# Kernel optimization log

Hardware: AMD Instinct MI355X
Metric: run time of the kernel (lower is better)

Reference implementation:

```python
import jax, jax.numpy as jnp
import numpy as np

D_IN = 1024
D_OUT = 1024
NUM_HEADS = 16
HEAD_DIM = D_OUT // NUM_HEADS

def setup_inputs() -> dict:
    key = jax.random.key(0)
    ks = jax.random.split(key, 6)
    b, t = 2, 2048
    s = 0.02
    return {
        "x": jax.random.normal(ks[0], (b, t, D_IN), dtype=jnp.float32),
        "Wq": jax.random.normal(ks[1], (D_IN, D_OUT), dtype=jnp.float32) * s,
        "Wk": jax.random.normal(ks[2], (D_IN, D_OUT), dtype=jnp.float32) * s,
        "Wv": jax.random.normal(ks[3], (D_IN, D_OUT), dtype=jnp.float32) * s,
        "Wo": jax.random.normal(ks[4], (D_OUT, D_OUT), dtype=jnp.float32) * s,
        "bo": jax.random.normal(ks[5], (D_OUT,), dtype=jnp.float32) * s,
    }

def reference(x, Wq, Wk, Wv, Wo, bo):
    b, t, _ = x.shape
    # QKV projections -> [b, h, t, d]
    def split_heads(y):
        return y.reshape(b, t, NUM_HEADS, HEAD_DIM).transpose(0, 2, 1, 3)
    q = split_heads(x @ Wq)
    k = split_heads(x @ Wk)
    v = split_heads(x @ Wv)
    # scores [b, h, t, t], causal mask, softmax over keys
    scores = jnp.einsum('bhqd,bhkd->bhqk', q, k)
    causal = jnp.tril(jnp.ones((t, t), dtype=bool))  # True where allowed
    scores = jnp.where(causal, scores, -jnp.inf)
    attn = jax.nn.softmax(scores / jnp.sqrt(jnp.float32(HEAD_DIM)), axis=-1)
    ctx = jnp.einsum('bhqk,bhkd->bhqd', attn, v)
    ctx = ctx.transpose(0, 2, 1, 3).reshape(b, t, D_OUT)
    return ctx @ Wo + bo
```

## Files before the change

### kernel.cpp

```cpp
#include <hip/hip_runtime.h>
#include <hip/hip_bf16.h>
#include <cstdint>
#include <cstddef>


typedef __bf16 bf16_t;
typedef __bf16 bf16x2 __attribute__((ext_vector_type(2)));
typedef __bf16 bf16x8 __attribute__((ext_vector_type(8)));
typedef float  f32x4  __attribute__((ext_vector_type(4)));

#define B_SZ 2
#define T_SZ 2048
#define DIN  1024
#define NH   16
#define HD   64

#define SCL_Q (0.125f * 1.44269504088896f)

__device__ __forceinline__ void gld_lds16(const void* g, void* l) {
    __builtin_amdgcn_global_load_lds(
        (const __attribute__((address_space(1))) void*)g,
        (__attribute__((address_space(3))) void*)l,
        16, 0, 0);
}

__global__ __launch_bounds__(256) void cvt_x_kernel(const float* __restrict__ src,
                                                    bf16_t* __restrict__ dst) {
    int i = blockIdx.x * blockDim.x + threadIdx.x;
    size_t base = (size_t)i * 8;
    float4 a = *(const float4*)(src + base);
    float4 b = *(const float4*)(src + base + 4);
    bf16x8 v;
    v[0] = (bf16_t)a.x; v[1] = (bf16_t)a.y; v[2] = (bf16_t)a.z; v[3] = (bf16_t)a.w;
    v[4] = (bf16_t)b.x; v[5] = (bf16_t)b.y; v[6] = (bf16_t)b.z; v[7] = (bf16_t)b.w;
    *(bf16x8*)(dst + base) = v;
}

__global__ __launch_bounds__(256) void transpose_cvt_kernel(const float* __restrict__ src,
                                                            bf16_t* __restrict__ dst,
                                                            int R, int C) {
    __shared__ float tile[32][33];
    int c0 = blockIdx.x * 32, r0 = blockIdx.y * 32;
    int tx = threadIdx.x, ty = threadIdx.y;
#pragma unroll
    for (int i = 0; i < 32; i += 8)
        tile[ty + i][tx] = src[(size_t)(r0 + ty + i) * C + c0 + tx];
    __syncthreads();
#pragma unroll
    for (int i = 0; i < 32; i += 8)
        dst[(size_t)(c0 + ty + i) * R + r0 + tx] = (bf16_t)tile[tx][ty + i];
}

__device__ __forceinline__ void gemm_tile_body(const bf16_t* __restrict__ A,
                                               const bf16_t* __restrict__ Bt,
                                               int m0, int n0, int K,
                                               f32x4 acc[4][4],
                                               bf16_t* As, bf16_t* Bs) {
    const int tid  = threadIdx.x;
    const int lane = tid & 63;
    const int wave = tid >> 6;
    const int wr   = (wave >> 1) * 64;
    const int wc   = (wave & 1) * 64;

#pragma unroll
    for (int mi = 0; mi < 4; ++mi)
#pragma unroll
        for (int ni = 0; ni < 4; ++ni)
            acc[mi][ni] = (f32x4){0.f, 0.f, 0.f, 0.f};

    for (int k0 = 0; k0 < K; k0 += 32) {
#pragma unroll
        for (int c = 0; c < 2; ++c) {
            int fb = (wave * 2 + c) * 1024;
            int e  = (fb >> 1) + lane * 8;
            int r  = e >> 5;
            int kk = e & 31;
            gld_lds16(A  + (size_t)(m0 + r) * K + k0 + kk, (char*)As + fb);
            gld_lds16(Bt + (size_t)(n0 + r) * K + k0 + kk, (char*)Bs + fb);
        }
        __syncthreads();

        bf16x8 af[4], bfr[4];
#pragma unroll
        for (int mi = 0; mi < 4; ++mi)
            af[mi] = *(const bf16x8*)(As + (wr + mi * 16 + (lane & 15)) * 32 + ((lane >> 4) * 8));
#pragma unroll
        for (int ni = 0; ni < 4; ++ni)
            bfr[ni] = *(const bf16x8*)(Bs + (wc + ni * 16 + (lane & 15)) * 32 + ((lane >> 4) * 8));
#pragma unroll
        for (int mi = 0; mi < 4; ++mi)
#pragma unroll
            for (int ni = 0; ni < 4; ++ni)
                acc[mi][ni] = __builtin_amdgcn_mfma_f32_16x16x32_bf16(af[mi], bfr[ni], acc[mi][ni], 0, 0, 0);
        __syncthreads();
    }
}

__global__ __launch_bounds__(256, 2) void gemm_qkv_kernel(const bf16_t* __restrict__ A,
                                                          const bf16_t* __restrict__ Bt,
                                                          bf16_t* __restrict__ Qb,
                                                          bf16_t* __restrict__ Kb,
                                                          bf16_t* __restrict__ Vt) {
    __shared__ alignas(16) bf16_t As[128 * 32];
    __shared__ alignas(16) bf16_t Bs[128 * 32];
    const int nTn = 3072 / 128;
    int m0 = (blockIdx.x / nTn) * 128;
    int n0 = (blockIdx.x % nTn) * 128;
    f32x4 acc[4][4];
    gemm_tile_body(A, Bt, m0, n0, DIN, acc, As, Bs);

    const int lane = threadIdx.x & 63;
    const int wave = threadIdx.x >> 6;
    const int wr = (wave >> 1) * 64, wc = (wave & 1) * 64;
#pragma unroll
    for (int mi = 0; mi < 4; ++mi)
#pragma unroll
        for (int ni = 0; ni < 4; ++ni)
#pragma unroll
            for (int j = 0; j < 4; ++j) {
                int m = m0 + wr + mi * 16 + ((lane >> 4) * 4) + j;
                int n = n0 + wc + ni * 16 + (lane & 15);
                int b = m >> 11, t = m & 2047;
                int part = n >> 10, c = n & 1023;
                int h = c >> 6, d = c & 63;
                float av = acc[mi][ni][j];
                if (part == 0)
                    Qb[(((size_t)(b * NH + h) * T_SZ + t) << 6) + d] = (bf16_t)(av * SCL_Q);
                else if (part == 1)
                    Kb[(((size_t)(b * NH + h) * T_SZ + t) << 6) + d] = (bf16_t)av;
                else
                    Vt[((size_t)(b * NH + h) * HD + d) * T_SZ + t] = (bf16_t)av;
            }
}

__global__ __launch_bounds__(256, 3) void attn_kernel(const bf16_t* __restrict__ Qb,
                                                      const bf16_t* __restrict__ Kb,
                                                      const bf16_t* __restrict__ Vt,
                                                      bf16_t* __restrict__ ctx) {
    __shared__ alignas(16) bf16_t Ks[2][64 * 64];
    __shared__ alignas(16) bf16_t Vs[2][64 * 64];
    __shared__ alignas(16) bf16_t P_lds[4][16][72];

    const int raw = blockIdx.x;
    const int xcd = raw & 7;
    const int jj  = raw >> 3;
    const int bh  = xcd * 4 + (jj & 3);
    const int qt  = 31 - (jj >> 2);

    const int lane = threadIdx.x & 63;
    const int wave = threadIdx.x >> 6;

    const bf16_t* Qp = Qb + (size_t)bh * T_SZ * HD;
    const bf16_t* Kp = Kb + (size_t)bh * T_SZ * HD;
    const bf16_t* Vp = Vt + (size_t)bh * HD * T_SZ;

    const int q0 = qt * 64 + wave * 16;
    const int rgrp = lane >> 4;
    const int rcol = lane & 15;

    const int st_r  = (lane >> 3);
    const int st_sl = lane & 7;

    bf16x8 qa[2];
#pragma unroll
    for (int s = 0; s < 2; ++s)
        qa[s] = *(const bf16x8*)(Qp + (size_t)(q0 + rcol) * HD + s * 32 + rgrp * 8);

    f32x4 o[4];
#pragma unroll
    for (int di = 0; di < 4; ++di) o[di] = (f32x4){0.f, 0.f, 0.f, 0.f};
    float mrun = -__builtin_inff();
    float lrun = 0.f;

#define STAGE(BUF, KT)                                                          \
    {                                                                           \
        const int k0s = (KT) * 64;                                              \
        _Pragma("unroll")                                                       \
        for (int c = 0; c < 2; ++c) {                                           \
            int r0 = (wave * 2 + c) * 8;                                        \
            int r  = r0 + st_r;                                                 \
            int sl = st_sl ^ (r & 7);                                           \
            gld_lds16(Kp + (size_t)(k0s + r) * HD + sl * 8,                     \
                      (char*)&Ks[BUF][0] + r0 * 128);                           \
            gld_lds16(Vp + (size_t)r * T_SZ + k0s + sl * 8,                     \
                      (char*)&Vs[BUF][0] + r0 * 128);                           \
        }                                                                       \
    }

    STAGE(0, 0);
    __syncthreads();
    int buf = 0;

    for (int kt = 0; kt <= qt; ++kt) {
        if (kt < qt) STAGE(buf ^ 1, kt + 1);

        const char* Kb_l = (const char*)&Ks[buf][0];
        const char* Vb_l = (const char*)&Vs[buf][0];

        f32x4 s_acc[4];
#pragma unroll
        for (int ni = 0; ni < 4; ++ni) s_acc[ni] = (f32x4){0.f, 0.f, 0.f, 0.f};
#pragma unroll
        for (int s = 0; s < 2; ++s)
#pragma unroll
            for (int ni = 0; ni < 4; ++ni) {
                int fr = ni * 16 + rcol;
                bf16x8 kb = *(const bf16x8*)(Kb_l + fr * 128 + (((s * 4 + rgrp) ^ (fr & 7)) << 4));
                s_acc[ni] = __builtin_amdgcn_mfma_f32_16x16x32_bf16(kb, qa[s], s_acc[ni], 0, 0, 0);
            }

        bf16x8 vf[2][4];
#pragma unroll
        for (int s = 0; s < 2; ++s)
#pragma unroll
            for (int di = 0; di < 4; ++di) {
                int fv = di * 16 + rcol;
                vf[s][di] = *(const bf16x8*)(Vb_l + fv * 128 + (((s * 4 + rgrp) ^ (fv & 7)) << 4));
            }

        float ptile[4][4];
        float pmax = -__builtin_inff();
        if (kt == qt) {
            const int qabs = q0 + rcol;
#pragma unroll
            for (int ni = 0; ni < 4; ++ni)
#pragma unroll
                for (int j = 0; j < 4; ++j) {
                    int kidx = qt * 64 + ni * 16 + rgrp * 4 + j;
                    float v = s_acc[ni][j];
                    if (kidx > qabs) v = -__builtin_inff();
                    ptile[ni][j] = v;
                    pmax = fmaxf(pmax, v);
                }
        } else {
#pragma unroll
            for (int ni = 0; ni < 4; ++ni)
#pragma unroll
                for (int j = 0; j < 4; ++j) {
                    float v = s_acc[ni][j];
                    ptile[ni][j] = v;
                    pmax = fmaxf(pmax, v);
                }
        }
        pmax = fmaxf(pmax, __shfl_xor(pmax, 16));
        pmax = fmaxf(pmax, __shfl_xor(pmax, 32));

        const bool fullb = __any(pmax > mrun + 8.f);
        float a_self = 1.f;
        if (fullb) {
            float newm = fmaxf(mrun, pmax);
            a_self = exp2f(mrun - newm);
            mrun = newm;
        }
        float rsum = 0.f;
#pragma unroll
        for (int ni = 0; ni < 4; ++ni)
#pragma unroll
            for (int j = 0; j < 4; ++j) {
                float p = exp2f(ptile[ni][j] - mrun);
                ptile[ni][j] = p;
                rsum += p;
            }
        rsum += __shfl_xor(rsum, 16);
        rsum += __shfl_xor(rsum, 32);
        if (fullb) {
            lrun = lrun * a_self + rsum;
#pragma unroll
            for (int j = 0; j < 4; ++j) {
                float aj = __shfl(a_self, (lane & 48) | (rgrp * 4 + j));
#pragma unroll
                for (int di = 0; di < 4; ++di) o[di][j] *= aj;
            }
        } else {
            lrun += rsum;
        }

#pragma unroll
        for (int ni = 0; ni < 4; ++ni)
#pragma unroll
            for (int jp = 0; jp < 2; ++jp) {
                bf16x2 pk;
                pk[0] = (bf16_t)ptile[ni][2 * jp];
                pk[1] = (bf16_t)ptile[ni][2 * jp + 1];
                *(bf16x2*)&P_lds[wave][rcol][ni * 16 + rgrp * 4 + 2 * jp] = pk;
            }
#pragma unroll
        for (int s = 0; s < 2; ++s) {
            bf16x8 pa = *(const bf16x8*)(&P_lds[wave][rcol][s * 32 + rgrp * 8]);
#pragma unroll
            for (int di = 0; di < 4; ++di)
                o[di] = __builtin_amdgcn_mfma_f32_16x16x32_bf16(pa, vf[s][di], o[di], 0, 0, 0);
        }
        __syncthreads();
        buf ^= 1;
    }
#undef STAGE

    const int b = bh >> 4, h = bh & 15;
    float invl[4];
#pragma unroll
    for (int j = 0; j < 4; ++j) {
        float lj = __shfl(lrun, (lane & 48) | (rgrp * 4 + j));
        invl[j] = 1.f / lj;
    }
#pragma unroll
    for (int di = 0; di < 4; ++di)
#pragma unroll
        for (int j = 0; j < 4; ++j) {
            int q = q0 + rgrp * 4 + j;
            int d = di * 16 + rcol;
            ctx[((size_t)(b * T_SZ + q) * NH + h) * HD + d] = (bf16_t)(o[di][j] * invl[j]);
        }
}

__global__ __launch_bounds__(256, 2) void gemm_out_kernel(const bf16_t* __restrict__ A,
                                                          const bf16_t* __restrict__ Bt,
                                                          const float* __restrict__ bias,
                                                          float* __restrict__ out) {
    __shared__ alignas(16) bf16_t As[128 * 32];
    __shared__ alignas(16) bf16_t Bs[128 * 32];
    const int nTn = 1024 / 128;
    int m0 = (blockIdx.x / nTn) * 128;
    int n0 = (blockIdx.x % nTn) * 128;
    f32x4 acc[4][4];
    gemm_tile_body(A, Bt, m0, n0, DIN, acc, As, Bs);

    const int lane = threadIdx.x & 63;
    const int wave = threadIdx.x >> 6;
    const int wr = (wave >> 1) * 64, wc = (wave & 1) * 64;
#pragma unroll
    for (int mi = 0; mi < 4; ++mi)
#pragma unroll
        for (int ni = 0; ni < 4; ++ni) {
            int n = n0 + wc + ni * 16 + (lane & 15);
            float bv = bias[n];
#pragma unroll
            for (int j = 0; j < 4; ++j) {
                int m = m0 + wr + mi * 16 + ((lane >> 4) * 4) + j;
                out[(size_t)m * 1024 + n] = acc[mi][ni][j] + bv;
            }
        }
}

extern "C" void kernel_launch(void* const* d_in, const int* in_sizes, int n_in,
                              void* d_out, int out_size, void* d_ws, size_t ws_size,
                              hipStream_t stream) {
    const float* x  = (const float*)d_in[0];
    const float* Wq = (const float*)d_in[1];
    const float* Wk = (const float*)d_in[2];
    const float* Wv = (const float*)d_in[3];
    const float* Wo = (const float*)d_in[4];
    const float* bo = (const float*)d_in[5];
    float* out = (float*)d_out;

    char* ws = (char*)d_ws;
    bf16_t* x_bf   = (bf16_t*)(ws);
    bf16_t* Wqkv_t = (bf16_t*)(ws + ((size_t)8 << 20));
    bf16_t* Wo_t   = (bf16_t*)(ws + ((size_t)14 << 20));
    bf16_t* Qb     = (bf16_t*)(ws + ((size_t)16 << 20));
    bf16_t* Kb     = (bf16_t*)(ws + ((size_t)24 << 20));
    bf16_t* Vt     = (bf16_t*)(ws + ((size_t)32 << 20));
    bf16_t* ctx    = (bf16_t*)(ws + ((size_t)40 << 20));

    cvt_x_kernel<<<2048, 256, 0, stream>>>(x, x_bf);
    transpose_cvt_kernel<<<dim3(32, 32), dim3(32, 8), 0, stream>>>(Wq, Wqkv_t, 1024, 1024);
    transpose_cvt_kernel<<<dim3(32, 32), dim3(32, 8), 0, stream>>>(Wk, Wqkv_t + (size_t)1024 * 1024, 1024, 1024);
    transpose_cvt_kernel<<<dim3(32, 32), dim3(32, 8), 0, stream>>>(Wv, Wqkv_t + (size_t)2048 * 1024, 1024, 1024);
    transpose_cvt_kernel<<<dim3(32, 32), dim3(32, 8), 0, stream>>>(Wo, Wo_t, 1024, 1024);
    gemm_qkv_kernel<<<32 * 24, 256, 0, stream>>>(x_bf, Wqkv_t, Qb, Kb, Vt);
    attn_kernel<<<B_SZ * NH * 32, 256, 0, stream>>>(Qb, Kb, Vt, ctx);
    gemm_out_kernel<<<32 * 8, 256, 0, stream>>>(ctx, Wo_t, bo, out);
}
```

Before: 194.7 us.

## Fuse prep kernels, remap GEMM blocks per XCD, vectorize V stores, shrink out-GEMM tile

Merges the x conversion and four weight transpose launches into one prep kernel to cut launch overhead. Remaps the QKV and output GEMM block indices so that neighbouring tiles are grouped onto the same XCD, which should improve L2 reuse. Stores V-transpose outputs as 4-wide vectors instead of scalar scattered writes. Halves the output GEMM M tile to 64 rows, doubling its grid from 256 to 512 blocks and raising the occupancy bound to 3, so the 256 CUs are filled better at the cost of less reuse per tile.

After: 174.9 us. -10.2%, faster.

```diff
diff --git a/kernel.cpp b/kernel.cpp
--- a/kernel.cpp
+++ b/kernel.cpp
@@ -6,6 +6,7 @@
 
 typedef __bf16 bf16_t;
 typedef __bf16 bf16x2 __attribute__((ext_vector_type(2)));
+typedef __bf16 bf16x4 __attribute__((ext_vector_type(4)));
 typedef __bf16 bf16x8 __attribute__((ext_vector_type(8)));
 typedef float  f32x4  __attribute__((ext_vector_type(4)));
 
@@ -24,31 +25,41 @@
         16, 0, 0);
 }
 
-__global__ __launch_bounds__(256) void cvt_x_kernel(const float* __restrict__ src,
-                                                    bf16_t* __restrict__ dst) {
-    int i = blockIdx.x * blockDim.x + threadIdx.x;
-    size_t base = (size_t)i * 8;
-    float4 a = *(const float4*)(src + base);
-    float4 b = *(const float4*)(src + base + 4);
-    bf16x8 v;
-    v[0] = (bf16_t)a.x; v[1] = (bf16_t)a.y; v[2] = (bf16_t)a.z; v[3] = (bf16_t)a.w;
-    v[4] = (bf16_t)b.x; v[5] = (bf16_t)b.y; v[6] = (bf16_t)b.z; v[7] = (bf16_t)b.w;
-    *(bf16x8*)(dst + base) = v;
-}
-
-__global__ __launch_bounds__(256) void transpose_cvt_kernel(const float* __restrict__ src,
-                                                            bf16_t* __restrict__ dst,
-                                                            int R, int C) {
+__global__ __launch_bounds__(256) void prep_kernel(const float* __restrict__ x,
+                                                   bf16_t* __restrict__ x_bf,
+                                                   const float* __restrict__ Wq,
+                                                   const float* __restrict__ Wk,
+                                                   const float* __restrict__ Wv,
+                                                   const float* __restrict__ Wo,
+                                                   bf16_t* __restrict__ Wqkv_t,
+                                                   bf16_t* __restrict__ Wo_t) {
     __shared__ float tile[32][33];
-    int c0 = blockIdx.x * 32, r0 = blockIdx.y * 32;
-    int tx = threadIdx.x, ty = threadIdx.y;
+    const int bid = blockIdx.x;
+    const int tid = threadIdx.x;
+    if (bid < 2048) {
+        size_t base = ((size_t)bid * 256 + tid) * 8;
+        float4 a = *(const float4*)(x + base);
+        float4 b = *(const float4*)(x + base + 4);
+        bf16x8 v;
+        v[0] = (bf16_t)a.x; v[1] = (bf16_t)a.y; v[2] = (bf16_t)a.z; v[3] = (bf16_t)a.w;
+        v[4] = (bf16_t)b.x; v[5] = (bf16_t)b.y; v[6] = (bf16_t)b.z; v[7] = (bf16_t)b.w;
+        *(bf16x8*)(x_bf + base) = v;
+        return;
+    }
+    const int tb = bid - 2048;
+    const int w  = tb >> 10;
+    const int t2 = tb & 1023;
+    const int c0 = (t2 & 31) * 32, r0 = (t2 >> 5) * 32;
+    const float* src = (w == 0) ? Wq : (w == 1) ? Wk : (w == 2) ? Wv : Wo;
+    bf16_t* dst = (w < 3) ? (Wqkv_t + (size_t)w * 1024 * 1024) : Wo_t;
+    const int tx = tid & 31, ty = tid >> 5;
 #pragma unroll
     for (int i = 0; i < 32; i += 8)
-        tile[ty + i][tx] = src[(size_t)(r0 + ty + i) * C + c0 + tx];
+        tile[ty + i][tx] = src[(size_t)(r0 + ty + i) * 1024 + c0 + tx];
     __syncthreads();
 #pragma unroll
     for (int i = 0; i < 32; i += 8)
-        dst[(size_t)(c0 + ty + i) * R + r0 + tx] = (bf16_t)tile[tx][ty + i];
+        dst[(size_t)(c0 + ty + i) * 1024 + r0 + tx] = (bf16_t)tile[tx][ty + i];
 }
 
 __device__ __forceinline__ void gemm_tile_body(const bf16_t* __restrict__ A,
@@ -104,8 +115,9 @@
     __shared__ alignas(16) bf16_t As[128 * 32];
     __shared__ alignas(16) bf16_t Bs[128 * 32];
     const int nTn = 3072 / 128;
-    int m0 = (blockIdx.x / nTn) * 128;
-    int n0 = (blockIdx.x % nTn) * 128;
+    const int bid = (blockIdx.x & 7) * 96 + (blockIdx.x >> 3);
+    int m0 = (bid / nTn) * 128;
+    int n0 = (bid % nTn) * 128;
     f32x4 acc[4][4];
     gemm_tile_body(A, Bt, m0, n0, DIN, acc, As, Bs);
 
@@ -115,22 +127,29 @@
 #pragma unroll
     for (int mi = 0; mi < 4; ++mi)
 #pragma unroll
-        for (int ni = 0; ni < 4; ++ni)
-#pragma unroll
-            for (int j = 0; j < 4; ++j) {
-                int m = m0 + wr + mi * 16 + ((lane >> 4) * 4) + j;
-                int n = n0 + wc + ni * 16 + (lane & 15);
-                int b = m >> 11, t = m & 2047;
-                int part = n >> 10, c = n & 1023;
-                int h = c >> 6, d = c & 63;
-                float av = acc[mi][ni][j];
-                if (part == 0)
-                    Qb[(((size_t)(b * NH + h) * T_SZ + t) << 6) + d] = (bf16_t)(av * SCL_Q);
-                else if (part == 1)
-                    Kb[(((size_t)(b * NH + h) * T_SZ + t) << 6) + d] = (bf16_t)av;
-                else
-                    Vt[((size_t)(b * NH + h) * HD + d) * T_SZ + t] = (bf16_t)av;
-            }
+        for (int ni = 0; ni < 4; ++ni) {
+            int t0 = m0 + wr + mi * 16 + ((lane >> 4) * 4);
+            int n  = n0 + wc + ni * 16 + (lane & 15);
+            int b  = t0 >> 11, tl = t0 & 2047;
+            int part = n >> 10, c = n & 1023;
+            int h = c >> 6, d = c & 63;
+            if (part == 2) {
+                bf16x4 pv;
+#pragma unroll
+                for (int j = 0; j < 4; ++j) pv[j] = (bf16_t)acc[mi][ni][j];
+                *(bf16x4*)&Vt[((size_t)(b * NH + h) * HD + d) * T_SZ + tl] = pv;
+            } else if (part == 0) {
+#pragma unroll
+                for (int j = 0; j < 4; ++j)
+                    Qb[(((size_t)(b * NH + h) * T_SZ + tl + j) << 6) + d] =
+                        (bf16_t)(acc[mi][ni][j] * SCL_Q);
+            } else {
+#pragma unroll
+                for (int j = 0; j < 4; ++j)
+                    Kb[(((size_t)(b * NH + h) * T_SZ + tl + j) << 6) + d] =
+                        (bf16_t)acc[mi][ni][j];
+            }
+        }
 }
 
 __global__ __launch_bounds__(256, 3) void attn_kernel(const bf16_t* __restrict__ Qb,
@@ -313,23 +332,65 @@
         }
 }
 
-__global__ __launch_bounds__(256, 2) void gemm_out_kernel(const bf16_t* __restrict__ A,
+__global__ __launch_bounds__(256, 3) void gemm_out_kernel(const bf16_t* __restrict__ A,
                                                           const bf16_t* __restrict__ Bt,
                                                           const float* __restrict__ bias,
                                                           float* __restrict__ out) {
-    __shared__ alignas(16) bf16_t As[128 * 32];
+    __shared__ alignas(16) bf16_t As[64 * 32];
     __shared__ alignas(16) bf16_t Bs[128 * 32];
     const int nTn = 1024 / 128;
-    int m0 = (blockIdx.x / nTn) * 128;
-    int n0 = (blockIdx.x % nTn) * 128;
-    f32x4 acc[4][4];
-    gemm_tile_body(A, Bt, m0, n0, DIN, acc, As, Bs);
-
-    const int lane = threadIdx.x & 63;
-    const int wave = threadIdx.x >> 6;
-    const int wr = (wave >> 1) * 64, wc = (wave & 1) * 64;
-#pragma unroll
-    for (int mi = 0; mi < 4; ++mi)
+    const int bid = (blockIdx.x & 7) * 64 + (blockIdx.x >> 3);
+    int m0 = (bid / nTn) * 64;
+    int n0 = (bid % nTn) * 128;
+
+    const int tid  = threadIdx.x;
+    const int lane = tid & 63;
+    const int wave = tid >> 6;
+    const int wr   = (wave >> 1) * 32;
+    const int wc   = (wave & 1) * 64;
+
+    f32x4 acc[2][4];
+#pragma unroll
+    for (int mi = 0; mi < 2; ++mi)
+#pragma unroll
+        for (int ni = 0; ni < 4; ++ni)
+            acc[mi][ni] = (f32x4){0.f, 0.f, 0.f, 0.f};
+
+    for (int k0 = 0; k0 < DIN; k0 += 32) {
+        {
+            int fb = wave * 1024;
+            int e  = (fb >> 1) + lane * 8;
+            int r  = e >> 5;
+            int kk = e & 31;
+            gld_lds16(A + (size_t)(m0 + r) * DIN + k0 + kk, (char*)As + fb);
+        }
+#pragma unroll
+        for (int c = 0; c < 2; ++c) {
+            int fb = (wave * 2 + c) * 1024;
+            int e  = (fb >> 1) + lane * 8;
+            int r  = e >> 5;
+            int kk = e & 31;
+            gld_lds16(Bt + (size_t)(n0 + r) * DIN + k0 + kk, (char*)Bs + fb);
+        }
+        __syncthreads();
+
+        bf16x8 af[2], bfr[4];
+#pragma unroll
+        for (int mi = 0; mi < 2; ++mi)
+            af[mi] = *(const bf16x8*)(As + (wr + mi * 16 + (lane & 15)) * 32 + ((lane >> 4) * 8));
+#pragma unroll
+        for (int ni = 0; ni < 4; ++ni)
+            bfr[ni] = *(const bf16x8*)(Bs + (wc + ni * 16 + (lane & 15)) * 32 + ((lane >> 4) * 8));
+#pragma unroll
+        for (int mi = 0; mi < 2; ++mi)
+#pragma unroll
+            for (int ni = 0; ni < 4; ++ni)
+                acc[mi][ni] = __builtin_amdgcn_mfma_f32_16x16x32_bf16(af[mi], bfr[ni], acc[mi][ni], 0, 0, 0);
+        __syncthreads();
+    }
+
+#pragma unroll
+    for (int mi = 0; mi < 2; ++mi)
 #pragma unroll
         for (int ni = 0; ni < 4; ++ni) {
             int n = n0 + wc + ni * 16 + (lane & 15);
@@ -362,12 +423,8 @@
     bf16_t* Vt     = (bf16_t*)(ws + ((size_t)32 << 20));
     bf16_t* ctx    = (bf16_t*)(ws + ((size_t)40 << 20));
 
-    cvt_x_kernel<<<2048, 256, 0, stream>>>(x, x_bf);
-    transpose_cvt_kernel<<<dim3(32, 32), dim3(32, 8), 0, stream>>>(Wq, Wqkv_t, 1024, 1024);
-    transpose_cvt_kernel<<<dim3(32, 32), dim3(32, 8), 0, stream>>>(Wk, Wqkv_t + (size_t)1024 * 1024, 1024, 1024);
-    transpose_cvt_kernel<<<dim3(32, 32), dim3(32, 8), 0, stream>>>(Wv, Wqkv_t + (size_t)2048 * 1024, 1024, 1024);
-    transpose_cvt_kernel<<<dim3(32, 32), dim3(32, 8), 0, stream>>>(Wo, Wo_t, 1024, 1024);
+    prep_kernel<<<6144, 256, 0, stream>>>(x, x_bf, Wq, Wk, Wv, Wo, Wqkv_t, Wo_t);
     gemm_qkv_kernel<<<32 * 24, 256, 0, stream>>>(x_bf, Wqkv_t, Qb, Kb, Vt);
     attn_kernel<<<B_SZ * NH * 32, 256, 0, stream>>>(Qb, Kb, Vt, ctx);
-    gemm_out_kernel<<<32 * 8, 256, 0, stream>>>(ctx, Wo_t, bo, out);
-}
+    gemm_out_kernel<<<64 * 8, 256, 0, stream>>>(ctx, Wo_t, bo, out);
+}
```
